# Optimization experiments

Hardware: AMD Instinct MI355X
Metric: run time of the kernel (lower is better)

## Reference

```python
import jax, jax.numpy as jnp
import numpy as np

EPS = 1e-5

def conv2d(x, w, stride=1, padding=0, bias=None):
    out = jax.lax.conv_general_dilated(
        x, w, (stride, stride), [(padding, padding), (padding, padding)],
        dimension_numbers=('NCHW', 'OIHW', 'NCHW'))
    if bias is not None:
        out = out + bias[None, :, None, None]
    return out

def bn_relu(x, gamma, beta, mean, var):
    scale = gamma / jnp.sqrt(var + EPS)
    return jax.nn.relu(x * scale[None, :, None, None]
                       + (beta - mean * scale)[None, :, None, None])

def deform_conv(x, wp, bp, wc, ks, pad, stride):
    # Canonical DeformConv2d (v1, modulation=False) from pytorch-deform-conv-v2.
    b, c, H, W = x.shape
    N = ks * ks
    offset = conv2d(x, wp, stride=stride, padding=1, bias=bp)        # (b,2N,h,w)
    h, w = offset.shape[2], offset.shape[3]
    xp = jnp.pad(x, ((0, 0), (0, 0), (pad, pad), (pad, pad)))        # zero_padding
    Hp, Wp = H + 2 * pad, W + 2 * pad
    off = offset.transpose(0, 2, 3, 1)                               # (b,h,w,2N)
    rng = jnp.arange(-(ks - 1) // 2, (ks - 1) // 2 + 1, dtype=x.dtype)
    pnx, pny = jnp.meshgrid(rng, rng, indexing='ij')
    pnx, pny = pnx.reshape(-1), pny.reshape(-1)                      # (N,)
    p0x = jnp.arange(1, h * stride + 1, stride, dtype=x.dtype)       # torch starts at 1
    p0y = jnp.arange(1, w * stride + 1, stride, dtype=x.dtype)
    px = p0x[None, :, None, None] + pnx[None, None, None, :] + off[..., :N]  # (b,h,w,N)
    py = p0y[None, None, :, None] + pny[None, None, None, :] + off[..., N:]
    qx0 = jnp.floor(jax.lax.stop_gradient(px))
    qy0 = jnp.floor(jax.lax.stop_gradient(py))
    qx0c = jnp.clip(qx0, 0, Hp - 1).astype(jnp.int32)
    qx1c = jnp.clip(qx0 + 1, 0, Hp - 1).astype(jnp.int32)
    qy0c = jnp.clip(qy0, 0, Wp - 1).astype(jnp.int32)
    qy1c = jnp.clip(qy0 + 1, 0, Wp - 1).astype(jnp.int32)
    pxc = jnp.clip(px, 0, Hp - 1)
    pyc = jnp.clip(py, 0, Wp - 1)
    fx0 = qx0c.astype(x.dtype); fx1 = qx1c.astype(x.dtype)
    fy0 = qy0c.astype(x.dtype); fy1 = qy1c.astype(x.dtype)
    g_lt = (1 + (fx0 - pxc)) * (1 + (fy0 - pyc))
    g_rb = (1 - (fx1 - pxc)) * (1 - (fy1 - pyc))
    g_lb = (1 + (fx0 - pxc)) * (1 - (fy1 - pyc))
    g_rt = (1 - (fx1 - pxc)) * (1 + (fy0 - pyc))
    xf = xp.reshape(b, c, Hp * Wp)
    def gather(qx, qy):
        idx = (qx * Wp + qy).reshape(b, 1, h * w * N)
        return jnp.take_along_axis(xf, idx, axis=2).reshape(b, c, h, w, N)
    x_off = (g_lt[:, None] * gather(qx0c, qy0c)
             + g_rb[:, None] * gather(qx1c, qy1c)
             + g_lb[:, None] * gather(qx0c, qy1c)
             + g_rt[:, None] * gather(qx1c, qy0c))                   # (b,c,h,w,N)
    # stride=ks conv over the reshaped (h*ks, w*ks) map == einsum over sample slot n
    return jnp.einsum('bchwn,ocn->bohw', x_off, wc.reshape(wc.shape[0], c, N))

def setup_inputs() -> dict:
    key = jax.random.key(0)
    ks = iter(jax.random.split(key, 40))
    def nrm(shape, scale):
        return jax.random.normal(next(ks), shape, dtype=jnp.float32) * scale
    def he(shape):  # fan_in = prod of all but first dim
        return nrm(shape, float(np.sqrt(2.0 / np.prod(shape[1:]))))
    def bn(c):
        return (jnp.ones((c,), jnp.float32) + nrm((c,), 0.05),  # gamma
                nrm((c,), 0.05),                                 # beta
                nrm((c,), 0.1),                                  # running mean
                jax.random.uniform(next(ks), (c,), jnp.float32, 0.5, 1.5))  # var
    inp = {'x': jax.random.normal(next(ks), (256, 3, 32, 32), dtype=jnp.float32)}
    inp['w1'] = he((32, 3, 3, 3)); inp['b1'] = nrm((32,), 0.01)
    inp['g1'], inp['be1'], inp['m1'], inp['v1'] = bn(32)
    inp['wp2'] = nrm((18, 32, 3, 3), 0.01); inp['bp2'] = nrm((18,), 0.001)
    inp['wc2'] = he((64, 32, 3, 3))
    inp['g2'], inp['be2'], inp['m2'], inp['v2'] = bn(64)
    inp['wp3'] = nrm((18, 64, 3, 3), 0.01); inp['bp3'] = nrm((18,), 0.001)
    inp['wc3'] = he((128, 64, 3, 3))
    inp['g3'], inp['be3'], inp['m3'], inp['v3'] = bn(128)
    inp['wp4'] = nrm((18, 128, 3, 3), 0.01); inp['bp4'] = nrm((18,), 0.001)
    inp['wc4'] = he((128, 128, 3, 3))
    inp['g4'], inp['be4'], inp['m4'], inp['v4'] = bn(128)
    inp['wcls'] = nrm((100, 128), float(1.0 / np.sqrt(128)))
    inp['bcls'] = nrm((100,), 0.01)
    return inp

def reference(x, w1, b1, g1, be1, m1, v1,
              wp2, bp2, wc2, g2, be2, m2, v2,
              wp3, bp3, wc3, g3, be3, m3, v3,
              wp4, bp4, wc4, g4, be4, m4, v4,
              wcls, bcls):
    h = bn_relu(conv2d(x, w1, stride=1, padding=1, bias=b1), g1, be1, m1, v1)   # (b,32,32,32)
    h = bn_relu(deform_conv(h, wp2, bp2, wc2, 3, 1, 2), g2, be2, m2, v2)        # (b,64,16,16)
    h = bn_relu(deform_conv(h, wp3, bp3, wc3, 3, 1, 1), g3, be3, m3, v3)        # (b,128,16,16)
    h = bn_relu(deform_conv(h, wp4, bp4, wc4, 3, 1, 2), g4, be4, m4, v4)        # (b,128,8,8)
    h = jnp.mean(h, axis=(2, 3))                                                # avg_pool2d(8) -> (b,128)
    return h @ wcls.T + bcls[None, :]
```

## Files before the change

kernel.cpp:

```cpp
#include <hip/hip_runtime.h>
#include <math.h>

#define BN_EPS 1e-5f

typedef __attribute__((ext_vector_type(4))) float f4;
typedef __attribute__((ext_vector_type(4))) int i4v;
typedef __attribute__((ext_vector_type(8))) short short8;
typedef __attribute__((ext_vector_type(4))) float f32x4;

__device__ inline unsigned short f2bf(float f) {
    unsigned int u = __builtin_bit_cast(unsigned int, f);
    return (unsigned short)((u + 0x7FFFu + ((u >> 16) & 1u)) >> 16);
}
__device__ inline float blo(int u) { return __builtin_bit_cast(float, (int)(u << 16)); }
__device__ inline float bhi(int u) { return __builtin_bit_cast(float, (int)(u & 0xffff0000)); }
__device__ inline int pkbf(float a, float b) {
    unsigned ua = __builtin_bit_cast(unsigned, a);
    unsigned ub = __builtin_bit_cast(unsigned, b);
    ua = (ua + 0x7FFFu + ((ua >> 16) & 1u)) >> 16;
    ub = (ub + 0x7FFFu + ((ub >> 16) & 1u)) & 0xFFFF0000u;
    return (int)(ua | ub);
}

struct CvtSeg { const float* src; unsigned short* dst; int oreal, c, kpad, end; };
struct CvtArgs { CvtSeg s[7]; };

__global__ __launch_bounds__(256)
void cvt_all(CvtArgs a)
{
    int idx = blockIdx.x * 256 + threadIdx.x;
    int base = 0;
    #pragma unroll
    for (int i = 0; i < 7; ++i) {
        if (idx < a.s[i].end) {
            int local = idx - base;
            int kpad = a.s[i].kpad, c = a.s[i].c;
            int o = local / kpad, k = local - o * kpad;
            unsigned short val = 0;
            if (o < a.s[i].oreal && k < 9 * c) {
                int n = k / c, cc = k - n * c;
                val = f2bf(a.s[i].src[(o * c + cc) * 9 + n]);
            }
            a.s[i].dst[local] = val;
            return;
        }
        base = a.s[i].end;
    }
}

__global__ __launch_bounds__(256)
void conv1_tile(const float* __restrict__ x, const unsigned short* __restrict__ wq,
                const float* __restrict__ bias, const float* __restrict__ g,
                const float* __restrict__ be, const float* __restrict__ m,
                const float* __restrict__ v, unsigned short* __restrict__ out)
{
    __shared__ __align__(16) float img[3072];
    __shared__ __align__(16) unsigned short wt[32 * 40];
    __shared__ float scb[32], shb[32];
    const int tid = threadIdx.x;
    const int b = blockIdx.x >> 2;
    const int qtr = blockIdx.x & 3;
    if (tid < 32) {
        float sc = g[tid] * rsqrtf(v[tid] + BN_EPS);
        scb[tid] = sc;
        shb[tid] = be[tid] - m[tid] * sc + bias[tid] * sc;
    }
    *(ushort4*)&wt[(tid >> 3) * 40 + (tid & 7) * 4] =
        *(const ushort4*)(wq + (tid >> 3) * 32 + (tid & 7) * 4);
    const float* xb = x + (size_t)b * 3072;
    #pragma unroll
    for (int r = 0; r < 3; ++r) {
        int idx = r * 256 + tid;
        *(f4*)&img[idx * 4] = *(const f4*)(xb + idx * 4);
    }
    __syncthreads();
    const int wid = tid >> 6, lane = tid & 63, quad = lane >> 4, m16 = lane & 15;
    short8 af0 = *(const short8*)&wt[m16 * 40 + quad * 8];
    short8 af1 = *(const short8*)&wt[(16 + m16) * 40 + quad * 8];
    #pragma unroll
    for (int it = 0; it < 4; ++it) {
        int pix = qtr * 256 + it * 64 + wid * 16 + m16;
        int i = pix >> 5, j = pix & 31;
        short8 bfrag;
        #pragma unroll
        for (int jj = 0; jj < 8; ++jj) {
            int k = quad * 8 + jj;
            float val = 0.f;
            if (k < 27) {
                int n = k / 3, c = k - n * 3;
                int u = i - 1 + n / 3, vv = j - 1 + n % 3;
                if (u >= 0 && u < 32 && vv >= 0 && vv < 32)
                    val = img[c * 1024 + u * 32 + vv];
            }
            bfrag[jj] = (short)f2bf(val);
        }
        f32x4 a0 = {0.f,0.f,0.f,0.f}, a1 = {0.f,0.f,0.f,0.f};
        a0 = __builtin_amdgcn_mfma_f32_16x16x32_bf16(af0, bfrag, a0, 0, 0, 0);
        a1 = __builtin_amdgcn_mfma_f32_16x16x32_bf16(af1, bfrag, a1, 0, 0, 0);
        unsigned short* op = out + ((size_t)b * 1024 + pix) * 32;
        ushort4 s0, s1;
        #pragma unroll
        for (int rr = 0; rr < 4; ++rr) {
            int o0 = quad * 4 + rr, o1 = 16 + quad * 4 + rr;
            ((unsigned short*)&s0)[rr] = f2bf(fmaxf(fmaf(a0[rr], scb[o0], shb[o0]), 0.f));
            ((unsigned short*)&s1)[rr] = f2bf(fmaxf(fmaf(a1[rr], scb[o1], shb[o1]), 0.f));
        }
        *(ushort4*)(op + quad * 4) = s0;
        *(ushort4*)(op + 16 + quad * 4) = s1;
    }
}

template<int C, int OREAL, int OPAD, int H, int W, int OH, int OW, int S,
         int MTILE, bool DEF, bool BN>
__global__ __launch_bounds__(256, 4)
void dconv(const unsigned short* __restrict__ xact, const float* __restrict__ offp,
           const unsigned short* __restrict__ wq,
           const float* __restrict__ q0, const float* __restrict__ q1,
           const float* __restrict__ q2, const float* __restrict__ q3,
           void* __restrict__ outv)
{
    constexpr int K = C * 9;
    constexpr int KCH = C / 32;
    constexpr int OSPLIT = (OPAD >= 64) ? 4 : 2;
    constexpr int G = 4 / OSPLIT;
    constexpr int OT = OPAD / (16 * OSPLIT);
    constexpr int PW = MTILE / G;
    constexpr int ST = PW / 16;
    constexpr int CP = C + 8;
    constexpr int GL = C / 8;
    constexpr int NGRP = 256 / GL;
    constexpr int NT_ITER = MTILE / NGRP;
    constexpr int OHW = OH * OW;
    constexpr int HWC = H * W * C;
    constexpr int Hp = H + 2, Wp = W + 2;
    static_assert(MTILE % NGRP == 0 && PW % 16 == 0, "tiling");

    __shared__ __align__(16) unsigned short xo[2][MTILE * CP];
    __shared__ float scb[OPAD], shb[OPAD];

    const int tid = threadIdx.x;
    const int p0 = blockIdx.x * MTILE;

    if (BN) {
        for (int o = tid; o < OREAL; o += 256) {
            float sc = q0[o] * rsqrtf(q3[o] + BN_EPS);
            scb[o] = sc;
            shb[o] = q1[o] - q2[o] * sc;
        }
    } else {
        for (int o = tid; o < OREAL; o += 256) scb[o] = q0[o];
    }

    const int gl = tid % GL;
    const int grp = tid / GL;
    const int wid = tid >> 6, lane = tid & 63, quad = lane >> 4, m16 = lane & 15;
    const int og = wid % OSPLIT, pg = wid / OSPLIT;
    const int obase = og * OT * 16;
    const int pixbase = pg * PW;

    auto do_gather = [&](int n, int buf) {
        #pragma unroll
        for (int it = 0; it < NT_ITER; ++it) {
            const int pix = it * NGRP + grp;
            const int p = p0 + pix;
            const int b = p / OHW;
            const int rem = p % OHW;
            const int i = rem / OW, j = rem % OW;
            const unsigned short* xb = xact + (size_t)b * HWC + gl * 8;
            i4v R;
            if constexpr (DEF) {
                float ox = offp[((size_t)(b * 18 + n) * OH + i) * OW + j];
                float oy = offp[((size_t)(b * 18 + 9 + n) * OH + i) * OW + j];
                float px = (float)(i * S + n / 3) + ox;
                float py = (float)(j * S + n % 3) + oy;
                int qx0 = (int)floorf(px), qy0 = (int)floorf(py);
                int x0 = min(max(qx0, 0), Hp - 1), x1 = min(max(qx0 + 1, 0), Hp - 1);
                int y0 = min(max(qy0, 0), Wp - 1), y1 = min(max(qy0 + 1, 0), Wp - 1);
                float pxc = fminf(fmaxf(px, 0.f), (float)(Hp - 1));
                float pyc = fminf(fmaxf(py, 0.f), (float)(Wp - 1));
                float gx0 = 1.f + ((float)x0 - pxc), gx1 = 1.f - ((float)x1 - pxc);
                float gy0 = 1.f + ((float)y0 - pyc), gy1 = 1.f - ((float)y1 - pyc);
                int u0 = x0 - 1, u1 = x1 - 1, v0 = y0 - 1, v1 = y1 - 1;
                bool k0 = (u0 >= 0 && u0 < H && v0 >= 0 && v0 < W);
                bool k1 = (u1 >= 0 && u1 < H && v1 >= 0 && v1 < W);
                bool k2 = (u0 >= 0 && u0 < H && v1 >= 0 && v1 < W);
                bool k3 = (u1 >= 0 && u1 < H && v0 >= 0 && v0 < W);
                int t0 = k0 ? (u0 * W + v0) * C : 0;  float w0 = k0 ? gx0 * gy0 : 0.f;
                int t1 = k1 ? (u1 * W + v1) * C : 0;  float w1 = k1 ? gx1 * gy1 : 0.f;
                int t2 = k2 ? (u0 * W + v1) * C : 0;  float w2 = k2 ? gx0 * gy1 : 0.f;
                int t3 = k3 ? (u1 * W + v0) * C : 0;  float w3 = k3 ? gx1 * gy0 : 0.f;
                i4v A = *(const i4v*)(xb + t0);
                i4v Bv = *(const i4v*)(xb + t1);
                i4v Cv = *(const i4v*)(xb + t2);
                i4v Dv = *(const i4v*)(xb + t3);
                #pragma unroll
                for (int e = 0; e < 4; ++e) {
                    float lo = w0 * blo(A[e]);
                    lo = fmaf(w1, blo(Bv[e]), lo);
                    lo = fmaf(w2, blo(Cv[e]), lo);
                    lo = fmaf(w3, blo(Dv[e]), lo);
                    float hi = w0 * bhi(A[e]);
                    hi = fmaf(w1, bhi(Bv[e]), hi);
                    hi = fmaf(w2, bhi(Cv[e]), hi);
                    hi = fmaf(w3, bhi(Dv[e]), hi);
                    R[e] = pkbf(lo, hi);
                }
            } else {
                int u = i * S - 1 + n / 3, vv = j * S - 1 + n % 3;
                bool ok = (u >= 0 && u < H && vv >= 0 && vv < W);
                if (ok) R = *(const i4v*)(xb + (u * W + vv) * C);
                else    R = (i4v){0, 0, 0, 0};
            }
            *(i4v*)&xo[buf][pix * CP + gl * 8] = R;
        }
    };

    auto load_wf = [&](int n, short8 (*wf)[OT]) {
        #pragma unroll
        for (int ch = 0; ch < KCH; ++ch)
            #pragma unroll
            for (int t = 0; t < OT; ++t)
                wf[ch][t] = *(const short8*)(wq + (size_t)(obase + t * 16 + m16) * K
                                             + n * C + ch * 32 + quad * 8);
    };

    f32x4 acc[ST][OT];
    #pragma unroll
    for (int st = 0; st < ST; ++st)
        #pragma unroll
        for (int t = 0; t < OT; ++t) acc[st][t] = (f32x4){0.f, 0.f, 0.f, 0.f};

    short8 wfA[KCH][OT], wfB[KCH][OT];
    do_gather(0, 0);
    load_wf(0, wfA);
    __syncthreads();

    for (int n = 0; n < 9; ++n) {
        const int cur = n & 1;
        if (n < 8) {
            do_gather(n + 1, cur ^ 1);
            load_wf(n + 1, wfB);
        }
        #pragma unroll
        for (int ch = 0; ch < KCH; ++ch)
            #pragma unroll
            for (int st = 0; st < ST; ++st) {
                short8 bf = *(const short8*)&xo[cur][(pixbase + st * 16 + m16) * CP
                                                    + ch * 32 + quad * 8];
                #pragma unroll
                for (int t = 0; t < OT; ++t)
                    acc[st][t] = __builtin_amdgcn_mfma_f32_16x16x32_bf16(
                        wfA[ch][t], bf, acc[st][t], 0, 0, 0);
            }
        if (n < 8) {
            #pragma unroll
            for (int ch = 0; ch < KCH; ++ch)
                #pragma unroll
                for (int t = 0; t < OT; ++t) wfA[ch][t] = wfB[ch][t];
        }
        __syncthreads();
    }

    if constexpr (BN) {
        unsigned short* outw = (unsigned short*)outv;
        #pragma unroll
        for (int st = 0; st < ST; ++st) {
            const int p = p0 + pixbase + st * 16 + m16;
            #pragma unroll
            for (int t = 0; t < OT; ++t) {
                int o = obase + t * 16 + quad * 4;
                ushort4 s;
                #pragma unroll
                for (int rr = 0; rr < 4; ++rr)
                    ((unsigned short*)&s)[rr] =
                        f2bf(fmaxf(fmaf(acc[st][t][rr], scb[o + rr], shb[o + rr]), 0.f));
                *(ushort4*)(outw + (size_t)p * OPAD + o) = s;
            }
        }
    } else {
        float* outf = (float*)outv;
        #pragma unroll
        for (int st = 0; st < ST; ++st) {
            const int p = p0 + pixbase + st * 16 + m16;
            const int b = p / OHW, rem = p % OHW;
            const int i = rem / OW, j = rem % OW;
            #pragma unroll
            for (int t = 0; t < OT; ++t)
                #pragma unroll
                for (int rr = 0; rr < 4; ++rr) {
                    int o = obase + t * 16 + quad * 4 + rr;
                    if (o < OREAL)
                        outf[((size_t)(b * 18 + o) * OH + i) * OW + j] =
                            acc[st][t][rr] + scb[o];
                }
        }
    }
}

__global__ __launch_bounds__(128)
void pool_fc(const unsigned short* __restrict__ h4, const float* __restrict__ wcls,
             const float* __restrict__ bcls, float* __restrict__ out)
{
    __shared__ float pool[128];
    int b = blockIdx.x;
    int tid = threadIdx.x;
    const unsigned short* src = h4 + (size_t)b * 8192;
    float s = 0.f;
    #pragma unroll
    for (int t = 0; t < 64; ++t)
        s += __builtin_bit_cast(float, (unsigned)src[t * 128 + tid] << 16);
    pool[tid] = s * (1.f / 64.f);
    __syncthreads();
    if (tid < 100) {
        float acc = bcls[tid];
        const float* wr = wcls + tid * 128;
        #pragma unroll
        for (int c = 0; c < 128; ++c) acc = fmaf(pool[c], wr[c], acc);
        out[(size_t)b * 100 + tid] = acc;
    }
}

extern "C" void kernel_launch(void* const* d_in, const int* in_sizes, int n_in,
                              void* d_out, int out_size, void* d_ws, size_t ws_size,
                              hipStream_t stream)
{
    const float* x    = (const float*)d_in[0];
    const float* w1   = (const float*)d_in[1];
    const float* b1   = (const float*)d_in[2];
    const float* g1   = (const float*)d_in[3];
    const float* be1  = (const float*)d_in[4];
    const float* m1   = (const float*)d_in[5];
    const float* v1   = (const float*)d_in[6];
    const float* wp2  = (const float*)d_in[7];
    const float* bp2  = (const float*)d_in[8];
    const float* wc2  = (const float*)d_in[9];
    const float* g2   = (const float*)d_in[10];
    const float* be2  = (const float*)d_in[11];
    const float* m2   = (const float*)d_in[12];
    const float* v2   = (const float*)d_in[13];
    const float* wp3  = (const float*)d_in[14];
    const float* bp3  = (const float*)d_in[15];
    const float* wc3  = (const float*)d_in[16];
    const float* g3   = (const float*)d_in[17];
    const float* be3  = (const float*)d_in[18];
    const float* m3   = (const float*)d_in[19];
    const float* v3   = (const float*)d_in[20];
    const float* wp4  = (const float*)d_in[21];
    const float* bp4  = (const float*)d_in[22];
    const float* wc4  = (const float*)d_in[23];
    const float* g4   = (const float*)d_in[24];
    const float* be4  = (const float*)d_in[25];
    const float* m4   = (const float*)d_in[26];
    const float* v4   = (const float*)d_in[27];
    const float* wcls = (const float*)d_in[28];
    const float* bcls = (const float*)d_in[29];
    float* out = (float*)d_out;

    float* ws  = (float*)d_ws;
    float* off = ws;
    unsigned short* h1 = (unsigned short*)(off + 1179648);
    unsigned short* h2 = h1 + 8388608;
    unsigned short* h3 = h2 + 4194304;
    unsigned short* h4 = h3 + 8388608;
    unsigned short* wc2b = h4 + 2097152;
    unsigned short* wc3b = wc2b + 18432;
    unsigned short* wc4b = wc3b + 73728;
    unsigned short* wp2b = wc4b + 147456;
    unsigned short* wp3b = wp2b + 9216;
    unsigned short* wp4b = wp3b + 18432;
    unsigned short* wq1  = wp4b + 36864;
    (void)ws_size; (void)in_sizes; (void)n_in; (void)out_size;

    CvtArgs ca;
    ca.s[0] = { wc2, wc2b, 64, 32, 288, 18432 };
    ca.s[1] = { wc3, wc3b, 128, 64, 576, 92160 };
    ca.s[2] = { wc4, wc4b, 128, 128, 1152, 239616 };
    ca.s[3] = { wp2, wp2b, 18, 32, 288, 248832 };
    ca.s[4] = { wp3, wp3b, 18, 64, 576, 267264 };
    ca.s[5] = { wp4, wp4b, 18, 128, 1152, 304128 };
    ca.s[6] = { w1, wq1, 32, 3, 32, 305152 };
    cvt_all<<<1192, 256, 0, stream>>>(ca);

    conv1_tile<<<1024, 256, 0, stream>>>(x, wq1, b1, g1, be1, m1, v1, h1);

    dconv<32, 18, 32, 32, 32, 16, 16, 2, 64, false, false><<<1024, 256, 0, stream>>>(
        h1, nullptr, wp2b, bp2, nullptr, nullptr, nullptr, off);
    dconv<32, 64, 64, 32, 32, 16, 16, 2, 64, true, true><<<1024, 256, 0, stream>>>(
        h1, off, wc2b, g2, be2, m2, v2, h2);

    dconv<64, 18, 32, 16, 16, 16, 16, 1, 64, false, false><<<1024, 256, 0, stream>>>(
        h2, nullptr, wp3b, bp3, nullptr, nullptr, nullptr, off);
    dconv<64, 128, 128, 16, 16, 16, 16, 1, 64, true, true><<<1024, 256, 0, stream>>>(
        h2, off, wc3b, g3, be3, m3, v3, h3);

    dconv<128, 18, 32, 16, 16, 8, 8, 2, 32, false, false><<<512, 256, 0, stream>>>(
        h3, nullptr, wp4b, bp4, nullptr, nullptr, nullptr, off);
    dconv<128, 128, 128, 16, 16, 8, 8, 2, 32, true, true><<<512, 256, 0, stream>>>(
        h3, off, wc4b, g4, be4, m4, v4, h4);

    pool_fc<<<256, 128, 0, stream>>>(h4, wcls, bcls, out);
}
```

Before: 251.6 us.

## Precompute per-tile bilinear sampling tables in LDS and shrink pixel tiles

Each block now computes, once per pixel and kernel tap, the four gather offsets and bilinear weights (or the masked offset for regular conv) and stores them in shared memory. The gather loop then only reads these tables, so the address math is no longer repeated in every channel-lane thread. The offset tensor becomes pixel-major, giving contiguous reads. bf16 packing uses a cheaper perm-based round that no longer rounds ties to even. MTILE is reduced so more blocks launch. The trade-offs are extra LDS and a sync, plus a slightly different rounding.

New measurement: 281.1 us. 11.7% more time.

```diff
diff --git a/kernel.cpp b/kernel.cpp
--- a/kernel.cpp
+++ b/kernel.cpp
@@ -14,12 +14,10 @@
 }
 __device__ inline float blo(int u) { return __builtin_bit_cast(float, (int)(u << 16)); }
 __device__ inline float bhi(int u) { return __builtin_bit_cast(float, (int)(u & 0xffff0000)); }
-__device__ inline int pkbf(float a, float b) {
-    unsigned ua = __builtin_bit_cast(unsigned, a);
-    unsigned ub = __builtin_bit_cast(unsigned, b);
-    ua = (ua + 0x7FFFu + ((ua >> 16) & 1u)) >> 16;
-    ub = (ub + 0x7FFFu + ((ub >> 16) & 1u)) & 0xFFFF0000u;
-    return (int)(ua | ub);
+__device__ inline int pkbf_fast(float hi, float lo) {
+    unsigned uh = __builtin_bit_cast(unsigned, hi) + 0x8000u;
+    unsigned ul = __builtin_bit_cast(unsigned, lo) + 0x8000u;
+    return (int)__builtin_amdgcn_perm(uh, ul, 0x07060302u);
 }
 
 struct CvtSeg { const float* src; unsigned short* dst; int oreal, c, kpad, end; };
@@ -129,18 +127,23 @@
     constexpr int CP = C + 8;
     constexpr int GL = C / 8;
     constexpr int NGRP = 256 / GL;
-    constexpr int NT_ITER = MTILE / NGRP;
     constexpr int OHW = OH * OW;
     constexpr int HWC = H * W * C;
     constexpr int Hp = H + 2, Wp = W + 2;
-    static_assert(MTILE % NGRP == 0 && PW % 16 == 0, "tiling");
+    static_assert(PW % 16 == 0 && OT >= 1, "tiling");
 
     __shared__ __align__(16) unsigned short xo[2][MTILE * CP];
+    __shared__ __align__(16) i4v tab_i[DEF ? MTILE : 1][9];
+    __shared__ __align__(16) f4  tab_w[DEF ? MTILE : 1][9];
+    __shared__ int tab_o[DEF ? 1 : MTILE][9];
+    __shared__ int tab_m[DEF ? 1 : MTILE][9];
+    __shared__ int imgb[MTILE];
     __shared__ float scb[OPAD], shb[OPAD];
 
     const int tid = threadIdx.x;
     const int p0 = blockIdx.x * MTILE;
 
+    if (tid < MTILE) imgb[tid] = ((p0 + tid) / OHW) * HWC;
     if (BN) {
         for (int o = tid; o < OREAL; o += 256) {
             float sc = q0[o] * rsqrtf(q3[o] + BN_EPS);
@@ -149,6 +152,43 @@
         }
     } else {
         for (int o = tid; o < OREAL; o += 256) scb[o] = q0[o];
+    }
+
+    for (int e = tid; e < MTILE * 9; e += 256) {
+        int lp = e / 9, n = e % 9;
+        int p = p0 + lp;
+        int rem = p % OHW;
+        int i = rem / OW, j = rem % OW;
+        if constexpr (DEF) {
+            float ox = offp[(size_t)p * 18 + n];
+            float oy = offp[(size_t)p * 18 + 9 + n];
+            float px = (float)(i * S + n / 3) + ox;
+            float py = (float)(j * S + n % 3) + oy;
+            int qx0 = (int)floorf(px), qy0 = (int)floorf(py);
+            int x0 = min(max(qx0, 0), Hp - 1), x1 = min(max(qx0 + 1, 0), Hp - 1);
+            int y0 = min(max(qy0, 0), Wp - 1), y1 = min(max(qy0 + 1, 0), Wp - 1);
+            float pxc = fminf(fmaxf(px, 0.f), (float)(Hp - 1));
+            float pyc = fminf(fmaxf(py, 0.f), (float)(Wp - 1));
+            float gx0 = 1.f + ((float)x0 - pxc), gx1 = 1.f - ((float)x1 - pxc);
+            float gy0 = 1.f + ((float)y0 - pyc), gy1 = 1.f - ((float)y1 - pyc);
+            int u0 = x0 - 1, u1 = x1 - 1, v0 = y0 - 1, v1 = y1 - 1;
+            bool k0 = (u0 >= 0 && u0 < H && v0 >= 0 && v0 < W);
+            bool k1 = (u1 >= 0 && u1 < H && v1 >= 0 && v1 < W);
+            bool k2 = (u0 >= 0 && u0 < H && v1 >= 0 && v1 < W);
+            bool k3 = (u1 >= 0 && u1 < H && v0 >= 0 && v0 < W);
+            i4v ti; f4 tw;
+            ti[0] = k0 ? (u0 * W + v0) * C : 0;  tw[0] = k0 ? gx0 * gy0 : 0.f;
+            ti[1] = k1 ? (u1 * W + v1) * C : 0;  tw[1] = k1 ? gx1 * gy1 : 0.f;
+            ti[2] = k2 ? (u0 * W + v1) * C : 0;  tw[2] = k2 ? gx0 * gy1 : 0.f;
+            ti[3] = k3 ? (u1 * W + v0) * C : 0;  tw[3] = k3 ? gx1 * gy0 : 0.f;
+            tab_i[lp][n] = ti;
+            tab_w[lp][n] = tw;
+        } else {
+            int u = i * S - 1 + n / 3, vv = j * S - 1 + n % 3;
+            bool ok = (u >= 0 && u < H && vv >= 0 && vv < W);
+            tab_o[lp][n] = ok ? (u * W + vv) * C : 0;
+            tab_m[lp][n] = ok ? -1 : 0;
+        }
     }
 
     const int gl = tid % GL;
@@ -159,57 +199,33 @@
     const int pixbase = pg * PW;
 
     auto do_gather = [&](int n, int buf) {
-        #pragma unroll
-        for (int it = 0; it < NT_ITER; ++it) {
-            const int pix = it * NGRP + grp;
-            const int p = p0 + pix;
-            const int b = p / OHW;
-            const int rem = p % OHW;
-            const int i = rem / OW, j = rem % OW;
-            const unsigned short* xb = xact + (size_t)b * HWC + gl * 8;
+        for (int pix = grp; pix < MTILE; pix += NGRP) {
+            const unsigned short* xb = xact + imgb[pix] + gl * 8;
             i4v R;
             if constexpr (DEF) {
-                float ox = offp[((size_t)(b * 18 + n) * OH + i) * OW + j];
-                float oy = offp[((size_t)(b * 18 + 9 + n) * OH + i) * OW + j];
-                float px = (float)(i * S + n / 3) + ox;
-                float py = (float)(j * S + n % 3) + oy;
-                int qx0 = (int)floorf(px), qy0 = (int)floorf(py);
-                int x0 = min(max(qx0, 0), Hp - 1), x1 = min(max(qx0 + 1, 0), Hp - 1);
-                int y0 = min(max(qy0, 0), Wp - 1), y1 = min(max(qy0 + 1, 0), Wp - 1);
-                float pxc = fminf(fmaxf(px, 0.f), (float)(Hp - 1));
-                float pyc = fminf(fmaxf(py, 0.f), (float)(Wp - 1));
-                float gx0 = 1.f + ((float)x0 - pxc), gx1 = 1.f - ((float)x1 - pxc);
-                float gy0 = 1.f + ((float)y0 - pyc), gy1 = 1.f - ((float)y1 - pyc);
-                int u0 = x0 - 1, u1 = x1 - 1, v0 = y0 - 1, v1 = y1 - 1;
-                bool k0 = (u0 >= 0 && u0 < H && v0 >= 0 && v0 < W);
-                bool k1 = (u1 >= 0 && u1 < H && v1 >= 0 && v1 < W);
-                bool k2 = (u0 >= 0 && u0 < H && v1 >= 0 && v1 < W);
-                bool k3 = (u1 >= 0 && u1 < H && v0 >= 0 && v0 < W);
-                int t0 = k0 ? (u0 * W + v0) * C : 0;  float w0 = k0 ? gx0 * gy0 : 0.f;
-                int t1 = k1 ? (u1 * W + v1) * C : 0;  float w1 = k1 ? gx1 * gy1 : 0.f;
-                int t2 = k2 ? (u0 * W + v1) * C : 0;  float w2 = k2 ? gx0 * gy1 : 0.f;
-                int t3 = k3 ? (u1 * W + v0) * C : 0;  float w3 = k3 ? gx1 * gy0 : 0.f;
-                i4v A = *(const i4v*)(xb + t0);
-                i4v Bv = *(const i4v*)(xb + t1);
-                i4v Cv = *(const i4v*)(xb + t2);
-                i4v Dv = *(const i4v*)(xb + t3);
-                #pragma unroll
-                for (int e = 0; e < 4; ++e) {
-                    float lo = w0 * blo(A[e]);
-                    lo = fmaf(w1, blo(Bv[e]), lo);
-                    lo = fmaf(w2, blo(Cv[e]), lo);
-                    lo = fmaf(w3, blo(Dv[e]), lo);
-                    float hi = w0 * bhi(A[e]);
-                    hi = fmaf(w1, bhi(Bv[e]), hi);
-                    hi = fmaf(w2, bhi(Cv[e]), hi);
-                    hi = fmaf(w3, bhi(Dv[e]), hi);
-                    R[e] = pkbf(lo, hi);
+                i4v ti = tab_i[pix][n];
+                f4  tw = tab_w[pix][n];
+                i4v A  = *(const i4v*)(xb + ti[0]);
+                i4v Bv = *(const i4v*)(xb + ti[1]);
+                i4v Cv = *(const i4v*)(xb + ti[2]);
+                i4v Dv = *(const i4v*)(xb + ti[3]);
+                #pragma unroll
+                for (int e2 = 0; e2 < 4; ++e2) {
+                    float lo = tw[0] * blo(A[e2]);
+                    lo = fmaf(tw[1], blo(Bv[e2]), lo);
+                    lo = fmaf(tw[2], blo(Cv[e2]), lo);
+                    lo = fmaf(tw[3], blo(Dv[e2]), lo);
+                    float hi = tw[0] * bhi(A[e2]);
+                    hi = fmaf(tw[1], bhi(Bv[e2]), hi);
+                    hi = fmaf(tw[2], bhi(Cv[e2]), hi);
+                    hi = fmaf(tw[3], bhi(Dv[e2]), hi);
+                    R[e2] = pkbf_fast(hi, lo);
                 }
             } else {
-                int u = i * S - 1 + n / 3, vv = j * S - 1 + n % 3;
-                bool ok = (u >= 0 && u < H && vv >= 0 && vv < W);
-                if (ok) R = *(const i4v*)(xb + (u * W + vv) * C);
-                else    R = (i4v){0, 0, 0, 0};
+                int mask = tab_m[pix][n];
+                i4v A = *(const i4v*)(xb + tab_o[pix][n]);
+                #pragma unroll
+                for (int e2 = 0; e2 < 4; ++e2) R[e2] = A[e2] & mask;
             }
             *(i4v*)&xo[buf][pix * CP + gl * 8] = R;
         }
@@ -231,6 +247,7 @@
         for (int t = 0; t < OT; ++t) acc[st][t] = (f32x4){0.f, 0.f, 0.f, 0.f};
 
     short8 wfA[KCH][OT], wfB[KCH][OT];
+    __syncthreads();
     do_gather(0, 0);
     load_wf(0, wfA);
     __syncthreads();
@@ -282,16 +299,13 @@
         #pragma unroll
         for (int st = 0; st < ST; ++st) {
             const int p = p0 + pixbase + st * 16 + m16;
-            const int b = p / OHW, rem = p % OHW;
-            const int i = rem / OW, j = rem % OW;
             #pragma unroll
             for (int t = 0; t < OT; ++t)
                 #pragma unroll
                 for (int rr = 0; rr < 4; ++rr) {
                     int o = obase + t * 16 + quad * 4 + rr;
                     if (o < OREAL)
-                        outf[((size_t)(b * 18 + o) * OH + i) * OW + j] =
-                            acc[st][t][rr] + scb[o];
+                        outf[(size_t)p * 18 + o] = acc[st][t][rr] + scb[o];
                 }
         }
     }
@@ -383,19 +397,19 @@
 
     conv1_tile<<<1024, 256, 0, stream>>>(x, wq1, b1, g1, be1, m1, v1, h1);
 
-    dconv<32, 18, 32, 32, 32, 16, 16, 2, 64, false, false><<<1024, 256, 0, stream>>>(
+    dconv<32, 18, 32, 32, 32, 16, 16, 2, 32, false, false><<<2048, 256, 0, stream>>>(
         h1, nullptr, wp2b, bp2, nullptr, nullptr, nullptr, off);
-    dconv<32, 64, 64, 32, 32, 16, 16, 2, 64, true, true><<<1024, 256, 0, stream>>>(
+    dconv<32, 64, 64, 32, 32, 16, 16, 2, 32, true, true><<<2048, 256, 0, stream>>>(
         h1, off, wc2b, g2, be2, m2, v2, h2);
 
-    dconv<64, 18, 32, 16, 16, 16, 16, 1, 64, false, false><<<1024, 256, 0, stream>>>(
+    dconv<64, 18, 32, 16, 16, 16, 16, 1, 32, false, false><<<2048, 256, 0, stream>>>(
         h2, nullptr, wp3b, bp3, nullptr, nullptr, nullptr, off);
-    dconv<64, 128, 128, 16, 16, 16, 16, 1, 64, true, true><<<1024, 256, 0, stream>>>(
+    dconv<64, 128, 128, 16, 16, 16, 16, 1, 32, true, true><<<2048, 256, 0, stream>>>(
         h2, off, wc3b, g3, be3, m3, v3, h3);
 
     dconv<128, 18, 32, 16, 16, 8, 8, 2, 32, false, false><<<512, 256, 0, stream>>>(
         h3, nullptr, wp4b, bp4, nullptr, nullptr, nullptr, off);
-    dconv<128, 128, 128, 16, 16, 8, 8, 2, 32, true, true><<<512, 256, 0, stream>>>(
+    dconv<128, 128, 128, 16, 16, 8, 8, 2, 16, true, true><<<1024, 256, 0, stream>>>(
         h3, off, wc4b, g4, be4, m4, v4, h4);
 
     pool_fc<<<256, 128, 0, stream>>>(h4, wcls, bcls, out);
```
